# Kernel tuning notes

Measured on AMD Instinct MI355X. Metric: run time of the kernel, lower is better.

Reference implementation:

```python
import jax, jax.numpy as jnp
import numpy as np

B, S, D = 8, 1024, 1024  # module requires S == D for the k + w_bias broadcast
MAX_LEN = 1024


def setup_inputs() -> dict:
    key = jax.random.key(0)
    ks = jax.random.split(key, 10)
    scale = 0.02
    return {
        "x": jax.random.normal(ks[0], (B, S, D), dtype=jnp.float32),
        "wq_w": scale * jax.random.normal(ks[1], (D, D), dtype=jnp.float32),
        "wq_b": jnp.zeros((D,), dtype=jnp.float32),
        "wk_w": scale * jax.random.normal(ks[2], (D, D), dtype=jnp.float32),
        "wk_b": jnp.zeros((D,), dtype=jnp.float32),
        "wv_w": scale * jax.random.normal(ks[3], (D, D), dtype=jnp.float32),
        "wv_b": jnp.zeros((D,), dtype=jnp.float32),
        "w": 0.01 * jax.random.normal(ks[4], (MAX_LEN, MAX_LEN), dtype=jnp.float32),
        "out_w": scale * jax.random.normal(ks[5], (D, D), dtype=jnp.float32),
        "out_b": jnp.zeros((D,), dtype=jnp.float32),
    }


def reference(x, wq_w, wq_b, wk_w, wk_b, wv_w, wv_b, w, out_w, out_b):
    # torch nn.Linear: y = x @ W.T + b
    q = x @ wq_w.T + wq_b            # [B,S,D]
    k = x @ wk_w.T + wk_b            # [B,S,D]
    v = x @ wv_w.T + wv_b            # [B,S,D]
    seq_len = x.shape[1]
    w_bias = w[:seq_len, :seq_len][None]          # [1,S,S]
    # NB: original code broadcasts [B,S,D] + [1,S,S]; requires D == S.
    num = jnp.matmul(jnp.exp(k + w_bias), v)      # [B,S,D]
    den = jnp.matmul(jnp.exp(w_bias), jnp.exp(k)) # [B,S,D]
    y = jax.nn.sigmoid(q) * num / den
    return y @ out_w.T + out_b
```

## Files before the change

kernel.cpp:

```cpp
#include <hip/hip_runtime.h>
#include <hip/hip_bf16.h>


typedef float  f32x4  __attribute__((ext_vector_type(4)));
typedef short  short8 __attribute__((ext_vector_type(8)));
typedef __bf16 bf16x8 __attribute__((ext_vector_type(8)));

__device__ __forceinline__ ushort f2bf(float f){
  uint u = __builtin_bit_cast(uint, f);
  u += 0x7fffu + ((u >> 16) & 1u);
  return (ushort)(u >> 16);
}
__device__ __forceinline__ float bf2f(ushort u){
  uint v = ((uint)u) << 16;
  return __builtin_bit_cast(float, v);
}

__device__ __forceinline__ void gload16(const ushort* g, ushort* l){
  __builtin_amdgcn_global_load_lds(
      (const __attribute__((address_space(1))) void*)g,
      (__attribute__((address_space(3))) void*)l, 16, 0, 0);
}

__device__ __forceinline__ f32x4 mfma16(short8 a, short8 b, f32x4 c){
  return __builtin_amdgcn_mfma_f32_16x16x32_bf16(
      __builtin_bit_cast(bf16x8, a), __builtin_bit_cast(bf16x8, b), c, 0, 0, 0);
}

template<int EPI>
__global__ __launch_bounds__(256) void gemm_bt(
    const ushort* __restrict__ A0, long sA0,
    const ushort* __restrict__ B0, long sB0,
    void* __restrict__ C0, long sC0, const float* __restrict__ bias0,
    const ushort* __restrict__ A1, long sA1,
    const ushort* __restrict__ B1, long sB1,
    void* __restrict__ C1, long sC1, const float* __restrict__ bias1,
    int N, int K, int zsplit)
{
  __shared__ ushort As[128 * 64] __attribute__((aligned(16)));
  __shared__ ushort Bs[128 * 64] __attribute__((aligned(16)));

  const int nx = gridDim.x, ny = gridDim.y;
  const long nwg = (long)nx * ny * gridDim.z;
  const long lid = ((long)blockIdx.z * ny + blockIdx.y) * nx + blockIdx.x;
  const long q8 = nwg >> 3, r8 = nwg & 7;
  const long xcd = lid & 7, idx = lid >> 3;
  const long sid = (xcd < r8 ? xcd * (q8 + 1) : r8 * (q8 + 1) + (xcd - r8) * q8) + idx;
  const int bx = (int)(sid % nx);
  const long t1 = sid / nx;
  const int by = (int)(t1 % ny);
  const int bz = (int)(t1 / ny);

  const int tid  = threadIdx.x;
  const int lane = tid & 63;
  const int wid  = tid >> 6;
  const int wm   = wid >> 1;
  const int wn   = wid & 1;
  const long tileM = (long)by * 128;
  const long tileN = (long)bx * 128;

  const ushort* Ab; const ushort* Bb; void* Cb; const float* bias;
  if (bz < zsplit) {
    Ab = A0 + (long)bz * sA0; Bb = B0 + (long)bz * sB0;
    Cb = (char*)C0 + (long)bz * sC0 * (EPI ? 4 : 2); bias = bias0;
  } else {
    long z1 = bz - zsplit;
    Ab = A1 + z1 * sA1; Bb = B1 + z1 * sB1;
    Cb = (char*)C1 + z1 * sC1 * (EPI ? 4 : 2); bias = bias1;
  }
  Ab += tileM * K;
  Bb += tileN * K;

  long gOff[4]; int lOff[4];
#pragma unroll
  for (int j = 0; j < 4; ++j) {
    int chunk = j * 256 + tid;
    int row   = chunk >> 3;
    int c16   = (chunk & 7) ^ (row & 7);
    gOff[j]   = (long)row * K + c16 * 8;
    lOff[j]   = chunk * 8;
  }

  f32x4 acc[4][4];
#pragma unroll
  for (int i = 0; i < 4; ++i)
#pragma unroll
    for (int j = 0; j < 4; ++j) acc[i][j] = (f32x4)0.f;

  const int rA0 = wm * 64 + (lane & 15);
  const int rB0 = wn * 64 + (lane & 15);
  const int cw0 = lane >> 4;

  for (int kt = 0; kt < K; kt += 64) {
    __syncthreads();
#pragma unroll
    for (int j = 0; j < 4; ++j) {
      gload16(Ab + gOff[j] + kt, &As[lOff[j]]);
      gload16(Bb + gOff[j] + kt, &Bs[lOff[j]]);
    }
    __syncthreads();

    short8 af[4][2], bf[4][2];
#pragma unroll
    for (int f = 0; f < 4; ++f) {
      int ra = rA0 + f * 16;
      int rb = rB0 + f * 16;
#pragma unroll
      for (int kk = 0; kk < 2; ++kk) {
        af[f][kk] = *(const short8*)&As[ra * 64 + (((kk * 4 + cw0) ^ (ra & 7)) * 8)];
        bf[f][kk] = *(const short8*)&Bs[rb * 64 + (((kk * 4 + cw0) ^ (rb & 7)) * 8)];
      }
    }
#pragma unroll
    for (int kk = 0; kk < 2; ++kk)
#pragma unroll
      for (int fi = 0; fi < 4; ++fi)
#pragma unroll
        for (int fj = 0; fj < 4; ++fj)
          acc[fi][fj] = mfma16(af[fi][kk], bf[fj][kk], acc[fi][fj]);
  }

#pragma unroll
  for (int fi = 0; fi < 4; ++fi) {
    long gm0 = tileM + wm * 64 + fi * 16 + (lane >> 4) * 4;
#pragma unroll
    for (int fj = 0; fj < 4; ++fj) {
      long gn = tileN + wn * 64 + fj * 16 + (lane & 15);
      float bv = bias ? bias[gn] : 0.f;
      if (EPI == 0) {
        ushort* Cp = (ushort*)Cb;
#pragma unroll
        for (int r = 0; r < 4; ++r)
          Cp[(gm0 + r) * (long)N + gn] = f2bf(acc[fi][fj][r] + bv);
      } else {
        float* Cp = (float*)Cb;
#pragma unroll
        for (int r = 0; r < 4; ++r)
          Cp[(gm0 + r) * (long)N + gn] = acc[fi][fj][r] + bv;
      }
    }
  }
}

__global__ void prep_all(const float* __restrict__ x,
                         const float* __restrict__ wq, const float* __restrict__ wk,
                         const float* __restrict__ wv, const float* __restrict__ ow,
                         const float* __restrict__ w,
                         const float* __restrict__ bq, const float* __restrict__ bk,
                         const float* __restrict__ bv,
                         ushort* __restrict__ xb,
                         ushort* __restrict__ wcat, ushort* __restrict__ owb,
                         ushort* __restrict__ ewb, float* __restrict__ bcat)
{
  const long MB = 1048576;
  long i4 = ((long)blockIdx.x * 256 + threadIdx.x) * 4;
  if (i4 < 8 * MB) {
    float4 v = *(const float4*)&x[i4];
    ushort4 o; o.x=f2bf(v.x); o.y=f2bf(v.y); o.z=f2bf(v.z); o.w=f2bf(v.w);
    *(ushort4*)&xb[i4] = o;
    return;
  }
  long j4 = i4 - 8 * MB;
  if (j4 < 3 * MB) {
    const float* src = (j4 < MB) ? wq : (j4 < 2 * MB ? wk : wv);
    long off = j4 & (MB - 1);
    float4 v = *(const float4*)&src[off];
    ushort4 o; o.x=f2bf(v.x); o.y=f2bf(v.y); o.z=f2bf(v.z); o.w=f2bf(v.w);
    *(ushort4*)&wcat[j4] = o;
  } else if (j4 < 4 * MB) {
    long off = j4 - 3 * MB;
    float4 v = *(const float4*)&ow[off];
    ushort4 o; o.x=f2bf(v.x); o.y=f2bf(v.y); o.z=f2bf(v.z); o.w=f2bf(v.w);
    *(ushort4*)&owb[off] = o;
  } else if (j4 < 5 * MB) {
    long off = j4 - 4 * MB;
    float4 v = *(const float4*)&w[off];
    ushort4 o;
    o.x=f2bf(expf(v.x)); o.y=f2bf(expf(v.y)); o.z=f2bf(expf(v.z)); o.w=f2bf(expf(v.w));
    *(ushort4*)&ewb[off] = o;
  } else {
    long i = j4 - 5 * MB;
    if (i < 3072) {
      const float* src = (i < 1024) ? bq : (i < 2048 ? bk : bv);
      long off = i & 1023;
      *(float4*)&bcat[i] = *(const float4*)&src[off];
    }
  }
}

__global__ void mid(const ushort* __restrict__ qkv, const float* __restrict__ w,
                    ushort* __restrict__ E, ushort* __restrict__ vT,
                    ushort* __restrict__ EKT)
{
  __shared__ float tk[32][33];
  __shared__ float tv[32][33];
  int b  = blockIdx.z;
  int s0 = blockIdx.y * 32, d0 = blockIdx.x * 32;
  int tx = threadIdx.x, ty = threadIdx.y;
#pragma unroll
  for (int i = 0; i < 4; ++i) {
    int s = s0 + ty + i * 8;
    long base = ((long)(b * 1024 + s)) * 3072;
    float kf = bf2f(qkv[base + 1024 + d0 + tx]);
    float vf = bf2f(qkv[base + 2048 + d0 + tx]);
    tk[ty + i * 8][tx] = expf(kf);
    tv[ty + i * 8][tx] = vf;
    float wv = w[(long)s * 1024 + d0 + tx];
    E[((long)(b * 1024 + s)) * 1024 + d0 + tx] = f2bf(expf(kf + wv));
  }
  __syncthreads();
#pragma unroll
  for (int i = 0; i < 4; ++i) {
    int d = d0 + ty + i * 8;
    long o = ((long)b * 1024 + d) * 1024 + s0 + tx;
    EKT[o] = f2bf(tk[tx][ty + i * 8]);
    vT [o] = f2bf(tv[tx][ty + i * 8]);
  }
}

__global__ void ew_y(const ushort* __restrict__ qkv, const ushort* __restrict__ num,
                     const ushort* __restrict__ den, ushort* __restrict__ y)
{
  long e4 = ((long)blockIdx.x * 256 + threadIdx.x) * 4;
  long m = e4 >> 10;
  int  d = (int)(e4 & 1023);
  ushort4 q4 = *(const ushort4*)&qkv[m * 3072 + d];
  ushort4 n4 = *(const ushort4*)&num[e4];
  ushort4 d4 = *(const ushort4*)&den[e4];
  ushort4 o;
  { float qv = bf2f(q4.x), s = 1.f / (1.f + expf(-qv)); o.x = f2bf(s * bf2f(n4.x) / bf2f(d4.x)); }
  { float qv = bf2f(q4.y), s = 1.f / (1.f + expf(-qv)); o.y = f2bf(s * bf2f(n4.y) / bf2f(d4.y)); }
  { float qv = bf2f(q4.z), s = 1.f / (1.f + expf(-qv)); o.z = f2bf(s * bf2f(n4.z) / bf2f(d4.z)); }
  { float qv = bf2f(q4.w), s = 1.f / (1.f + expf(-qv)); o.w = f2bf(s * bf2f(n4.w) / bf2f(d4.w)); }
  *(ushort4*)&y[e4] = o;
}

extern "C" void kernel_launch(void* const* d_in, const int* in_sizes, int n_in,
                              void* d_out, int out_size, void* d_ws, size_t ws_size,
                              hipStream_t stream)
{
  const float* x     = (const float*)d_in[0];
  const float* wq_w  = (const float*)d_in[1];
  const float* wq_b  = (const float*)d_in[2];
  const float* wk_w  = (const float*)d_in[3];
  const float* wk_b  = (const float*)d_in[4];
  const float* wv_w  = (const float*)d_in[5];
  const float* wv_b  = (const float*)d_in[6];
  const float* w     = (const float*)d_in[7];
  const float* out_w = (const float*)d_in[8];
  const float* out_b = (const float*)d_in[9];
  float* out = (float*)d_out;

  const long MB = 1048576;
  char* ws = (char*)d_ws;
  size_t o = 0;
  auto alloc = [&](size_t bytes){ size_t r = o; o += (bytes + 255) & ~(size_t)255; return r; };

  ushort* xb   = (ushort*)(ws + alloc(8192 * 1024 * 2));
  ushort* wcat = (ushort*)(ws + alloc(3072 * 1024 * 2));
  ushort* owb  = (ushort*)(ws + alloc(1024 * 1024 * 2));
  ushort* ewb  = (ushort*)(ws + alloc(1024 * 1024 * 2));
  float*  bcat = (float*) (ws + alloc(3072 * 4));
  ushort* qkvb = (ushort*)(ws + alloc(8192 * 3072 * 2));
  ushort* Eb   = (ushort*)(ws + alloc(8 * MB * 2));
  ushort* vTb  = (ushort*)(ws + alloc(8 * MB * 2));
  ushort* EKTb = (ushort*)(ws + alloc(8 * MB * 2));
  ushort* numb = (ushort*)(ws + alloc(8 * MB * 2));
  ushort* denb = (ushort*)(ws + alloc(8 * MB * 2));
  ushort* yb   = (ushort*)(ws + alloc(8 * MB * 2));
  (void)ws_size; (void)in_sizes; (void)n_in; (void)out_size;

  prep_all<<<13315, 256, 0, stream>>>(x, wq_w, wk_w, wv_w, out_w, w,
                                      wq_b, wk_b, wv_b,
                                      xb, wcat, owb, ewb, bcat);

  gemm_bt<0><<<dim3(24, 64, 1), 256, 0, stream>>>(
      xb, 0, wcat, 0, qkvb, 0, bcat,
      xb, 0, wcat, 0, qkvb, 0, bcat,
      3072, 1024, 1);

  mid<<<dim3(32, 32, 8), dim3(32, 8), 0, stream>>>(qkvb, w, Eb, vTb, EKTb);

  gemm_bt<0><<<dim3(8, 8, 16), 256, 0, stream>>>(
      Eb,  MB, vTb,  MB, numb, MB, nullptr,
      ewb, 0,  EKTb, MB, denb, MB, nullptr,
      1024, 1024, 8);

  ew_y<<<8192, 256, 0, stream>>>(qkvb, numb, denb, yb);

  gemm_bt<1><<<dim3(8, 64, 1), 256, 0, stream>>>(
      yb, 0, owb, 0, out, 0, out_b,
      yb, 0, owb, 0, out, 0, out_b,
      1024, 1024, 1);
}
```

Baseline: 288.1 us.

## Fuse exp epilogues into QKV GEMM and num/den GEMMs with gating epilogue

The QKV GEMM epilogue now writes q, exp(k) and exp(k+w) straight into separate buffers, so the mid kernel only transposes exp(k) and v, using wider 64x64 tiles. The num and den GEMMs are merged into one kernel that accumulates both in registers and applies sigmoid(q)*num/den in its epilogue, which removes the ew_y kernel and the bf16 round trip of num and den. This cuts launches and global memory traffic. The price is a fused kernel with double the accumulators and 64KB of LDS, and half as many workgroups (512), which lowers occupancy and parallelism.

```diff
diff --git a/kernel.cpp b/kernel.cpp
--- a/kernel.cpp
+++ b/kernel.cpp
@@ -27,30 +27,29 @@
       __builtin_bit_cast(bf16x8, a), __builtin_bit_cast(bf16x8, b), c, 0, 0, 0);
 }
 
-template<int EPI>
-__global__ __launch_bounds__(256) void gemm_bt(
-    const ushort* __restrict__ A0, long sA0,
-    const ushort* __restrict__ B0, long sB0,
-    void* __restrict__ C0, long sC0, const float* __restrict__ bias0,
-    const ushort* __restrict__ A1, long sA1,
-    const ushort* __restrict__ B1, long sB1,
-    void* __restrict__ C1, long sC1, const float* __restrict__ bias1,
-    int N, int K, int zsplit)
-{
-  __shared__ ushort As[128 * 64] __attribute__((aligned(16)));
-  __shared__ ushort Bs[128 * 64] __attribute__((aligned(16)));
-
+__device__ __forceinline__ void xcd_swz(int& bx, int& by, int& bz){
   const int nx = gridDim.x, ny = gridDim.y;
   const long nwg = (long)nx * ny * gridDim.z;
   const long lid = ((long)blockIdx.z * ny + blockIdx.y) * nx + blockIdx.x;
   const long q8 = nwg >> 3, r8 = nwg & 7;
   const long xcd = lid & 7, idx = lid >> 3;
   const long sid = (xcd < r8 ? xcd * (q8 + 1) : r8 * (q8 + 1) + (xcd - r8) * q8) + idx;
-  const int bx = (int)(sid % nx);
+  bx = (int)(sid % nx);
   const long t1 = sid / nx;
-  const int by = (int)(t1 % ny);
-  const int bz = (int)(t1 / ny);
-
+  by = (int)(t1 % ny);
+  bz = (int)(t1 / ny);
+}
+
+__global__ __launch_bounds__(256) void gemm_qkv(
+    const ushort* __restrict__ A, const ushort* __restrict__ B,
+    const float* __restrict__ bias, const float* __restrict__ w,
+    ushort* __restrict__ qb, ushort* __restrict__ kb,
+    ushort* __restrict__ Eb, ushort* __restrict__ vb)
+{
+  __shared__ ushort As[128 * 64] __attribute__((aligned(16)));
+  __shared__ ushort Bs[128 * 64] __attribute__((aligned(16)));
+
+  int bx, by, bz; xcd_swz(bx, by, bz); (void)bz;
   const int tid  = threadIdx.x;
   const int lane = tid & 63;
   const int wid  = tid >> 6;
@@ -58,18 +57,10 @@
   const int wn   = wid & 1;
   const long tileM = (long)by * 128;
   const long tileN = (long)bx * 128;
-
-  const ushort* Ab; const ushort* Bb; void* Cb; const float* bias;
-  if (bz < zsplit) {
-    Ab = A0 + (long)bz * sA0; Bb = B0 + (long)bz * sB0;
-    Cb = (char*)C0 + (long)bz * sC0 * (EPI ? 4 : 2); bias = bias0;
-  } else {
-    long z1 = bz - zsplit;
-    Ab = A1 + z1 * sA1; Bb = B1 + z1 * sB1;
-    Cb = (char*)C1 + z1 * sC1 * (EPI ? 4 : 2); bias = bias1;
-  }
-  Ab += tileM * K;
-  Bb += tileN * K;
+  const int  seg   = (int)(tileN >> 10);
+
+  const ushort* Ab = A + tileM * 1024;
+  const ushort* Bb = B + tileN * 1024;
 
   long gOff[4]; int lOff[4];
 #pragma unroll
@@ -77,7 +68,7 @@
     int chunk = j * 256 + tid;
     int row   = chunk >> 3;
     int c16   = (chunk & 7) ^ (row & 7);
-    gOff[j]   = (long)row * K + c16 * 8;
+    gOff[j]   = (long)row * 1024 + c16 * 8;
     lOff[j]   = chunk * 8;
   }
 
@@ -91,7 +82,7 @@
   const int rB0 = wn * 64 + (lane & 15);
   const int cw0 = lane >> 4;
 
-  for (int kt = 0; kt < K; kt += 64) {
+  for (int kt = 0; kt < 1024; kt += 64) {
     __syncthreads();
 #pragma unroll
     for (int j = 0; j < 4; ++j) {
@@ -126,18 +117,204 @@
 #pragma unroll
     for (int fj = 0; fj < 4; ++fj) {
       long gn = tileN + wn * 64 + fj * 16 + (lane & 15);
-      float bv = bias ? bias[gn] : 0.f;
-      if (EPI == 0) {
-        ushort* Cp = (ushort*)Cb;
-#pragma unroll
-        for (int r = 0; r < 4; ++r)
-          Cp[(gm0 + r) * (long)N + gn] = f2bf(acc[fi][fj][r] + bv);
-      } else {
-        float* Cp = (float*)Cb;
-#pragma unroll
-        for (int r = 0; r < 4; ++r)
-          Cp[(gm0 + r) * (long)N + gn] = acc[fi][fj][r] + bv;
-      }
+      int  nl = (int)(gn & 1023);
+      float bv = bias[gn];
+#pragma unroll
+      for (int r = 0; r < 4; ++r) {
+        long m = gm0 + r;
+        float val = acc[fi][fj][r] + bv;
+        long o = m * 1024 + nl;
+        if (seg == 0) {
+          qb[o] = f2bf(val);
+        } else if (seg == 1) {
+          float wv = w[(long)(m & 1023) * 1024 + nl];
+          kb[o] = f2bf(expf(val));
+          Eb[o] = f2bf(expf(val + wv));
+        } else {
+          vb[o] = f2bf(val);
+        }
+      }
+    }
+  }
+}
+
+__global__ __launch_bounds__(256, 2) void gemm_nd(
+    const ushort* __restrict__ E,  const ushort* __restrict__ vT,
+    const ushort* __restrict__ ew, const ushort* __restrict__ EKT,
+    const ushort* __restrict__ qb, ushort* __restrict__ y)
+{
+  __shared__ ushort sh[4 * 8192] __attribute__((aligned(16)));
+
+  const long MB = 1048576;
+  int bx, by, bz; xcd_swz(bx, by, bz);
+  const int tid  = threadIdx.x;
+  const int lane = tid & 63;
+  const int wid  = tid >> 6;
+  const int wm   = wid >> 1;
+  const int wn   = wid & 1;
+  const long tileM = (long)by * 128;
+  const long tileN = (long)bx * 128;
+  const long z = bz;
+
+  const ushort* Ae = E   + z * MB + tileM * 1024;
+  const ushort* Bv = vT  + z * MB + tileN * 1024;
+  const ushort* Aw = ew  +          tileM * 1024;
+  const ushort* Bk = EKT + z * MB + tileN * 1024;
+
+  long gOff[4]; int lOff[4];
+#pragma unroll
+  for (int j = 0; j < 4; ++j) {
+    int chunk = j * 256 + tid;
+    int row   = chunk >> 3;
+    int c16   = (chunk & 7) ^ (row & 7);
+    gOff[j]   = (long)row * 1024 + c16 * 8;
+    lOff[j]   = chunk * 8;
+  }
+
+  f32x4 accN[4][4], accD[4][4];
+#pragma unroll
+  for (int i = 0; i < 4; ++i)
+#pragma unroll
+    for (int j = 0; j < 4; ++j) { accN[i][j] = (f32x4)0.f; accD[i][j] = (f32x4)0.f; }
+
+  const int rA0 = wm * 64 + (lane & 15);
+  const int rB0 = wn * 64 + (lane & 15);
+  const int cw0 = lane >> 4;
+
+  for (int kt = 0; kt < 1024; kt += 64) {
+    __syncthreads();
+#pragma unroll
+    for (int j = 0; j < 4; ++j) {
+      gload16(Ae + gOff[j] + kt, &sh[lOff[j]]);
+      gload16(Bv + gOff[j] + kt, &sh[8192  + lOff[j]]);
+      gload16(Aw + gOff[j] + kt, &sh[16384 + lOff[j]]);
+      gload16(Bk + gOff[j] + kt, &sh[24576 + lOff[j]]);
+    }
+    __syncthreads();
+
+#pragma unroll
+    for (int kk = 0; kk < 2; ++kk) {
+      short8 a[4], b[4];
+#pragma unroll
+      for (int f = 0; f < 4; ++f) {
+        int ra = rA0 + f * 16, rb = rB0 + f * 16;
+        a[f] = *(const short8*)&sh[ra * 64 + (((kk * 4 + cw0) ^ (ra & 7)) * 8)];
+        b[f] = *(const short8*)&sh[8192 + rb * 64 + (((kk * 4 + cw0) ^ (rb & 7)) * 8)];
+      }
+#pragma unroll
+      for (int fi = 0; fi < 4; ++fi)
+#pragma unroll
+        for (int fj = 0; fj < 4; ++fj)
+          accN[fi][fj] = mfma16(a[fi], b[fj], accN[fi][fj]);
+#pragma unroll
+      for (int f = 0; f < 4; ++f) {
+        int ra = rA0 + f * 16, rb = rB0 + f * 16;
+        a[f] = *(const short8*)&sh[16384 + ra * 64 + (((kk * 4 + cw0) ^ (ra & 7)) * 8)];
+        b[f] = *(const short8*)&sh[24576 + rb * 64 + (((kk * 4 + cw0) ^ (rb & 7)) * 8)];
+      }
+#pragma unroll
+      for (int fi = 0; fi < 4; ++fi)
+#pragma unroll
+        for (int fj = 0; fj < 4; ++fj)
+          accD[fi][fj] = mfma16(a[fi], b[fj], accD[fi][fj]);
+    }
+  }
+
+#pragma unroll
+  for (int fi = 0; fi < 4; ++fi) {
+    long gm0 = tileM + wm * 64 + fi * 16 + (lane >> 4) * 4;
+#pragma unroll
+    for (int fj = 0; fj < 4; ++fj) {
+      long gn = tileN + wn * 64 + fj * 16 + (lane & 15);
+#pragma unroll
+      for (int r = 0; r < 4; ++r) {
+        long idx = z * MB + (gm0 + r) * 1024 + gn;
+        float qv = bf2f(qb[idx]);
+        float s  = 1.f / (1.f + expf(-qv));
+        y[idx] = f2bf(s * accN[fi][fj][r] / accD[fi][fj][r]);
+      }
+    }
+  }
+}
+
+__global__ __launch_bounds__(256) void gemm_out(
+    const ushort* __restrict__ A, const ushort* __restrict__ B,
+    float* __restrict__ C, const float* __restrict__ bias)
+{
+  __shared__ ushort As[128 * 64] __attribute__((aligned(16)));
+  __shared__ ushort Bs[128 * 64] __attribute__((aligned(16)));
+
+  int bx, by, bz; xcd_swz(bx, by, bz); (void)bz;
+  const int tid  = threadIdx.x;
+  const int lane = tid & 63;
+  const int wid  = tid >> 6;
+  const int wm   = wid >> 1;
+  const int wn   = wid & 1;
+  const long tileM = (long)by * 128;
+  const long tileN = (long)bx * 128;
+
+  const ushort* Ab = A + tileM * 1024;
+  const ushort* Bb = B + tileN * 1024;
+
+  long gOff[4]; int lOff[4];
+#pragma unroll
+  for (int j = 0; j < 4; ++j) {
+    int chunk = j * 256 + tid;
+    int row   = chunk >> 3;
+    int c16   = (chunk & 7) ^ (row & 7);
+    gOff[j]   = (long)row * 1024 + c16 * 8;
+    lOff[j]   = chunk * 8;
+  }
+
+  f32x4 acc[4][4];
+#pragma unroll
+  for (int i = 0; i < 4; ++i)
+#pragma unroll
+    for (int j = 0; j < 4; ++j) acc[i][j] = (f32x4)0.f;
+
+  const int rA0 = wm * 64 + (lane & 15);
+  const int rB0 = wn * 64 + (lane & 15);
+  const int cw0 = lane >> 4;
+
+  for (int kt = 0; kt < 1024; kt += 64) {
+    __syncthreads();
+#pragma unroll
+    for (int j = 0; j < 4; ++j) {
+      gload16(Ab + gOff[j] + kt, &As[lOff[j]]);
+      gload16(Bb + gOff[j] + kt, &Bs[lOff[j]]);
+    }
+    __syncthreads();
+
+    short8 af[4][2], bf[4][2];
+#pragma unroll
+    for (int f = 0; f < 4; ++f) {
+      int ra = rA0 + f * 16;
+      int rb = rB0 + f * 16;
+#pragma unroll
+      for (int kk = 0; kk < 2; ++kk) {
+        af[f][kk] = *(const short8*)&As[ra * 64 + (((kk * 4 + cw0) ^ (ra & 7)) * 8)];
+        bf[f][kk] = *(const short8*)&Bs[rb * 64 + (((kk * 4 + cw0) ^ (rb & 7)) * 8)];
+      }
+    }
+#pragma unroll
+    for (int kk = 0; kk < 2; ++kk)
+#pragma unroll
+      for (int fi = 0; fi < 4; ++fi)
+#pragma unroll
+        for (int fj = 0; fj < 4; ++fj)
+          acc[fi][fj] = mfma16(af[fi][kk], bf[fj][kk], acc[fi][fj]);
+  }
+
+#pragma unroll
+  for (int fi = 0; fi < 4; ++fi) {
+    long gm0 = tileM + wm * 64 + fi * 16 + (lane >> 4) * 4;
+#pragma unroll
+    for (int fj = 0; fj < 4; ++fj) {
+      long gn = tileN + wn * 64 + fj * 16 + (lane & 15);
+      float bv = bias[gn];
+#pragma unroll
+      for (int r = 0; r < 4; ++r)
+        C[(gm0 + r) * 1024 + gn] = acc[fi][fj][r] + bv;
     }
   }
 }
@@ -188,51 +365,34 @@
   }
 }
 
-__global__ void mid(const ushort* __restrict__ qkv, const float* __restrict__ w,
-                    ushort* __restrict__ E, ushort* __restrict__ vT,
-                    ushort* __restrict__ EKT)
-{
-  __shared__ float tk[32][33];
-  __shared__ float tv[32][33];
-  int b  = blockIdx.z;
-  int s0 = blockIdx.y * 32, d0 = blockIdx.x * 32;
-  int tx = threadIdx.x, ty = threadIdx.y;
+__global__ void mid2(const ushort* __restrict__ kb, const ushort* __restrict__ vb,
+                     ushort* __restrict__ EKT, ushort* __restrict__ vT)
+{
+  __shared__ ushort t1[64][68];
+  __shared__ ushort t2[64][68];
+  const int b  = blockIdx.z;
+  const int s0 = blockIdx.y * 64, d0 = blockIdx.x * 64;
+  const int t  = threadIdx.x;
+  const int sl = t >> 4, q4 = (t & 15) * 4;
+  const long base = (long)b * 1048576;
 #pragma unroll
   for (int i = 0; i < 4; ++i) {
-    int s = s0 + ty + i * 8;
-    long base = ((long)(b * 1024 + s)) * 3072;
-    float kf = bf2f(qkv[base + 1024 + d0 + tx]);
-    float vf = bf2f(qkv[base + 2048 + d0 + tx]);
-    tk[ty + i * 8][tx] = expf(kf);
-    tv[ty + i * 8][tx] = vf;
-    float wv = w[(long)s * 1024 + d0 + tx];
-    E[((long)(b * 1024 + s)) * 1024 + d0 + tx] = f2bf(expf(kf + wv));
+    int s = sl + i * 16;
+    long src = base + (long)(s0 + s) * 1024 + d0 + q4;
+    *(ushort4*)&t1[s][q4] = *(const ushort4*)&kb[src];
+    *(ushort4*)&t2[s][q4] = *(const ushort4*)&vb[src];
   }
   __syncthreads();
 #pragma unroll
   for (int i = 0; i < 4; ++i) {
-    int d = d0 + ty + i * 8;
-    long o = ((long)b * 1024 + d) * 1024 + s0 + tx;
-    EKT[o] = f2bf(tk[tx][ty + i * 8]);
-    vT [o] = f2bf(tv[tx][ty + i * 8]);
-  }
-}
-
-__global__ void ew_y(const ushort* __restrict__ qkv, const ushort* __restrict__ num,
-                     const ushort* __restrict__ den, ushort* __restrict__ y)
-{
-  long e4 = ((long)blockIdx.x * 256 + threadIdx.x) * 4;
-  long m = e4 >> 10;
-  int  d = (int)(e4 & 1023);
-  ushort4 q4 = *(const ushort4*)&qkv[m * 3072 + d];
-  ushort4 n4 = *(const ushort4*)&num[e4];
-  ushort4 d4 = *(const ushort4*)&den[e4];
-  ushort4 o;
-  { float qv = bf2f(q4.x), s = 1.f / (1.f + expf(-qv)); o.x = f2bf(s * bf2f(n4.x) / bf2f(d4.x)); }
-  { float qv = bf2f(q4.y), s = 1.f / (1.f + expf(-qv)); o.y = f2bf(s * bf2f(n4.y) / bf2f(d4.y)); }
-  { float qv = bf2f(q4.z), s = 1.f / (1.f + expf(-qv)); o.z = f2bf(s * bf2f(n4.z) / bf2f(d4.z)); }
-  { float qv = bf2f(q4.w), s = 1.f / (1.f + expf(-qv)); o.w = f2bf(s * bf2f(n4.w) / bf2f(d4.w)); }
-  *(ushort4*)&y[e4] = o;
+    int d = sl + i * 16;
+    long dst = base + (long)(d0 + d) * 1024 + s0 + q4;
+    ushort4 o1, o2;
+    o1.x = t1[q4    ][d]; o1.y = t1[q4 + 1][d]; o1.z = t1[q4 + 2][d]; o1.w = t1[q4 + 3][d];
+    o2.x = t2[q4    ][d]; o2.y = t2[q4 + 1][d]; o2.z = t2[q4 + 2][d]; o2.w = t2[q4 + 3][d];
+    *(ushort4*)&EKT[dst] = o1;
+    *(ushort4*)&vT [dst] = o2;
+  }
 }
 
 extern "C" void kernel_launch(void* const* d_in, const int* in_sizes, int n_in,
@@ -256,17 +416,17 @@
   size_t o = 0;
   auto alloc = [&](size_t bytes){ size_t r = o; o += (bytes + 255) & ~(size_t)255; return r; };
 
-  ushort* xb   = (ushort*)(ws + alloc(8192 * 1024 * 2));
-  ushort* wcat = (ushort*)(ws + alloc(3072 * 1024 * 2));
-  ushort* owb  = (ushort*)(ws + alloc(1024 * 1024 * 2));
-  ushort* ewb  = (ushort*)(ws + alloc(1024 * 1024 * 2));
+  ushort* xb   = (ushort*)(ws + alloc(8 * MB * 2));
+  ushort* wcat = (ushort*)(ws + alloc(3 * MB * 2));
+  ushort* owb  = (ushort*)(ws + alloc(1 * MB * 2));
+  ushort* ewb  = (ushort*)(ws + alloc(1 * MB * 2));
   float*  bcat = (float*) (ws + alloc(3072 * 4));
-  ushort* qkvb = (ushort*)(ws + alloc(8192 * 3072 * 2));
+  ushort* qb   = (ushort*)(ws + alloc(8 * MB * 2));
+  ushort* kb   = (ushort*)(ws + alloc(8 * MB * 2));
   ushort* Eb   = (ushort*)(ws + alloc(8 * MB * 2));
+  ushort* vb   = (ushort*)(ws + alloc(8 * MB * 2));
   ushort* vTb  = (ushort*)(ws + alloc(8 * MB * 2));
   ushort* EKTb = (ushort*)(ws + alloc(8 * MB * 2));
-  ushort* numb = (ushort*)(ws + alloc(8 * MB * 2));
-  ushort* denb = (ushort*)(ws + alloc(8 * MB * 2));
   ushort* yb   = (ushort*)(ws + alloc(8 * MB * 2));
   (void)ws_size; (void)in_sizes; (void)n_in; (void)out_size;
 
@@ -274,22 +434,12 @@
                                       wq_b, wk_b, wv_b,
                                       xb, wcat, owb, ewb, bcat);
 
-  gemm_bt<0><<<dim3(24, 64, 1), 256, 0, stream>>>(
-      xb, 0, wcat, 0, qkvb, 0, bcat,
-      xb, 0, wcat, 0, qkvb, 0, bcat,
-      3072, 1024, 1);
-
-  mid<<<dim3(32, 32, 8), dim3(32, 8), 0, stream>>>(qkvb, w, Eb, vTb, EKTb);
-
-  gemm_bt<0><<<dim3(8, 8, 16), 256, 0, stream>>>(
-      Eb,  MB, vTb,  MB, numb, MB, nullptr,
-      ewb, 0,  EKTb, MB, denb, MB, nullptr,
-      1024, 1024, 8);
-
-  ew_y<<<8192, 256, 0, stream>>>(qkvb, numb, denb, yb);
-
-  gemm_bt<1><<<dim3(8, 64, 1), 256, 0, stream>>>(
-      yb, 0, owb, 0, out, 0, out_b,
-      yb, 0, owb, 0, out, 0, out_b,
-      1024, 1024, 1);
-}
+  gemm_qkv<<<dim3(24, 64, 1), 256, 0, stream>>>(
+      xb, wcat, bcat, w, qb, kb, Eb, vb);
+
+  mid2<<<dim3(16, 16, 8), 256, 0, stream>>>(kb, vb, EKTb, vTb);
+
+  gemm_nd<<<dim3(8, 8, 8), 256, 0, stream>>>(Eb, vTb, ewb, EKTb, qb, yb);
+
+  gemm_out<<<dim3(8, 64, 1), 256, 0, stream>>>(yb, owb, out, out_b);
+}
```

Result: slower. 297.1 us (+3.1%).
